# Optimization experiments

Measured on AMD Instinct MI355X. Metric: run time of the kernel, lower is better.

Reference implementation:

```python
import jax, jax.numpy as jnp
import numpy as np

HEADS = 16

def rotate_half(x):
    x1, x2 = jnp.split(x, 2, axis=-1)
    return jnp.concatenate((-x2, x1), axis=-1)

def setup_inputs() -> dict:
    key = jax.random.key(0)
    k1, k2, k3, k4 = jax.random.split(key, 4)
    b, n, h = 2, 2048, 1024
    d = h // HEADS
    x = jax.random.normal(k1, (b, n, h), dtype=jnp.float32)
    rotary_emb = jax.random.normal(k2, (n, d), dtype=jnp.float32)
    w_qkv = jax.random.normal(k3, (h, 3 * h), dtype=jnp.float32) * (1.0 / np.sqrt(h))
    w_out = jax.random.normal(k4, (h, h), dtype=jnp.float32) * (1.0 / np.sqrt(h))
    return {"x": x, "rotary_emb": rotary_emb, "w_qkv": w_qkv, "w_out": w_out}

def reference(x, rotary_emb, w_qkv, w_out):
    b, n, hidden = x.shape
    d = hidden // HEADS
    # fused QKV projection: [b,n,3*hidden]
    qkv = jnp.einsum('bnh,hk->bnk', x, w_qkv)
    q, k, v = jnp.split(qkv, 3, axis=-1)
    # [b,n,hidden] -> [b,H,n,d]
    split_heads = lambda t: t.reshape(b, n, HEADS, d).transpose(0, 2, 1, 3)
    q, k, v = split_heads(q), split_heads(k), split_heads(v)
    # rotary: pos is [n,d], broadcast over batch/heads
    cos = jnp.cos(rotary_emb)[None, None]
    sin = jnp.sin(rotary_emb)[None, None]
    q = q * cos + rotate_half(q) * sin
    k = k * cos + rotate_half(k) * sin
    # SDPA (no mask, no dropout)
    scale = 1.0 / np.sqrt(d).astype(np.float32)
    scores = jnp.einsum('bhqd,bhkd->bhqk', q, k) * scale
    attn = jax.nn.softmax(scores, axis=-1)
    out = jnp.einsum('bhqk,bhkd->bhqd', attn, v)
    out = out.transpose(0, 2, 1, 3).reshape(b, n, hidden)
    return jnp.einsum('bnh,hk->bnk', out, w_out)
```

## Files before the change

kernel.cpp:

```cpp
#include <hip/hip_runtime.h>
#include <math.h>

#define HEADS 16
#define DH    64
#define SEQ   2048
#define HID   1024
#define NROW  4096

typedef __attribute__((ext_vector_type(8))) short bf16x8;
typedef __attribute__((ext_vector_type(4))) float f32x4;

#define AS1 __attribute__((address_space(1)))
#define AS3 __attribute__((address_space(3)))

#define QSCALE 0.18033688011112042f

__device__ __forceinline__ unsigned short f2bf(float x) {
    unsigned int u = __builtin_bit_cast(unsigned int, x);
    u = (u + 0x7FFFu + ((u >> 16) & 1u)) >> 16;
    return (unsigned short)u;
}

__device__ __forceinline__ void gload_lds16(const unsigned short* g, unsigned short* l) {
    __builtin_amdgcn_global_load_lds((AS1 void*)g, (AS3 void*)l, 16, 0, 0);
}

__device__ void wtrans_body(const float* __restrict__ wsrc, unsigned short* __restrict__ wt,
                            int K, int N, int bx, int by, float (*T)[65])
{
    const int tid = threadIdx.x;
    const int k0 = by * 64, n0 = bx * 64;
    #pragma unroll
    for (int rnd = 0; rnd < 4; ++rnd) {
        int row = (tid >> 4) + rnd * 16;
        int c = (tid & 15) * 4;
        float4 v = *(const float4*)&wsrc[(size_t)(k0 + row) * N + n0 + c];
        T[row][c] = v.x; T[row][c+1] = v.y; T[row][c+2] = v.z; T[row][c+3] = v.w;
    }
    __syncthreads();
    const int sr = tid >> 3, sc = (tid & 7) << 3;
    #pragma unroll
    for (int half = 0; half < 2; ++half) {
        int n = sr + half * 32;
        union { unsigned short u[8]; bf16x8 v; } pk;
        #pragma unroll
        for (int j = 0; j < 8; ++j) pk.u[j] = f2bf(T[sc + j][n]);
        *(bf16x8*)&wt[(size_t)(n0 + n) * K + k0 + sc] = pk.v;
    }
}

__global__ __launch_bounds__(256) void prep(const float* __restrict__ x,
                                            const float* __restrict__ rot,
                                            const float* __restrict__ w_qkv,
                                            const float* __restrict__ w_out,
                                            unsigned short* __restrict__ xb,
                                            float2* __restrict__ ctab,
                                            unsigned short* __restrict__ wqkvT,
                                            unsigned short* __restrict__ woutT)
{
    __shared__ float T[64][65];
    const int bid = blockIdx.x;
    if (bid < 2048) {
        size_t i = ((size_t)bid * 256 + threadIdx.x) * 8;
        float4 a = *(const float4*)&x[i];
        float4 b = *(const float4*)&x[i + 4];
        union { unsigned short u[8]; bf16x8 v; } pk;
        pk.u[0] = f2bf(a.x); pk.u[1] = f2bf(a.y); pk.u[2] = f2bf(a.z); pk.u[3] = f2bf(a.w);
        pk.u[4] = f2bf(b.x); pk.u[5] = f2bf(b.y); pk.u[6] = f2bf(b.z); pk.u[7] = f2bf(b.w);
        *(bf16x8*)&xb[i] = pk.v;
    } else if (bid < 2560) {
        int i = (bid - 2048) * 256 + threadIdx.x;
        float r = rot[i];
        float s, c;
        __sincosf(r, &s, &c);
        ctab[i] = make_float2(c, s);
    } else if (bid < 3328) {
        int idx = bid - 2560;
        wtrans_body(w_qkv, wqkvT, 1024, 3072, idx % 48, idx / 48, T);
    } else {
        int idx = bid - 3328;
        wtrans_body(w_out, woutT, 1024, 1024, idx % 16, idx / 16, T);
    }
}

__global__ __launch_bounds__(256) void gemm_qkv(const unsigned short* __restrict__ A,
                                                const unsigned short* __restrict__ Bt,
                                                const float2* __restrict__ ctab,
                                                unsigned short* __restrict__ qb,
                                                unsigned short* __restrict__ kb,
                                                unsigned short* __restrict__ vt)
{
    __shared__ __align__(16) unsigned short As[128 * 32];
    __shared__ __align__(16) unsigned short Bs[128 * 32];
    const int tid = threadIdx.x;
    const int w = tid >> 6, lane = tid & 63;
    const int quad = lane >> 4, lm = lane & 15;
    const int wr = (w >> 1) * 64, wc = (w & 1) * 64;
    const int bm = blockIdx.y * 128, bn = blockIdx.x * 128;
    const int m0 = tid >> 2;
    const int sk = (tid & 3) << 3;

    f32x4 acc[4][4];
    #pragma unroll
    for (int i = 0; i < 4; ++i)
        #pragma unroll
        for (int j = 0; j < 4; ++j) acc[i][j] = (f32x4){0.f, 0.f, 0.f, 0.f};

    for (int k0 = 0; k0 < 1024; k0 += 32) {
        __syncthreads();
        gload_lds16(&A [(size_t)(bm + m0     ) * 1024 + k0 + sk], As + (size_t)w * 512);
        gload_lds16(&A [(size_t)(bm + m0 + 64) * 1024 + k0 + sk], As + 2048 + (size_t)w * 512);
        gload_lds16(&Bt[(size_t)(bn + m0     ) * 1024 + k0 + sk], Bs + (size_t)w * 512);
        gload_lds16(&Bt[(size_t)(bn + m0 + 64) * 1024 + k0 + sk], Bs + 2048 + (size_t)w * 512);
        __syncthreads();
        bf16x8 af[4], bfr[4];
        #pragma unroll
        for (int mt = 0; mt < 4; ++mt) af[mt] = *(const bf16x8*)&As[(wr + mt * 16 + lm) * 32 + quad * 8];
        #pragma unroll
        for (int nt = 0; nt < 4; ++nt) bfr[nt] = *(const bf16x8*)&Bs[(wc + nt * 16 + lm) * 32 + quad * 8];
        #pragma unroll
        for (int mt = 0; mt < 4; ++mt)
            #pragma unroll
            for (int nt = 0; nt < 4; ++nt)
                acc[mt][nt] = __builtin_amdgcn_mfma_f32_16x16x32_bf16(af[mt], bfr[nt], acc[mt][nt], 0, 0, 0);
    }

    const int colbase = bn + wc;
    const int region = colbase >> 10;
    const int h = (colbase >> 6) & 15;

    if (region == 2) {
        #pragma unroll
        for (int mt = 0; mt < 4; ++mt) {
            int rowb = bm + wr + mt * 16 + quad * 4;
            int b = rowb >> 11, seq = rowb & (SEQ - 1);
            int t = seq >> 5, ks = seq & 31;
            #pragma unroll
            for (int nt = 0; nt < 4; ++nt) {
                int d = nt * 16 + lm;
                ushort4 pk;
                pk.x = f2bf(acc[mt][nt][0]); pk.y = f2bf(acc[mt][nt][1]);
                pk.z = f2bf(acc[mt][nt][2]); pk.w = f2bf(acc[mt][nt][3]);
                *(ushort4*)&vt[(((size_t)(b * HEADS + h) * 64 + t) * 64 + d) * 32 + ks] = pk;
            }
        }
    } else {
        const float qs = (region == 0) ? QSCALE : 1.0f;
        unsigned short* dst = (region == 0) ? qb : kb;
        #pragma unroll
        for (int mt = 0; mt < 4; ++mt) {
            #pragma unroll
            for (int nt = 0; nt < 2; ++nt) {
                int d = nt * 16 + lm;
                #pragma unroll
                for (int r = 0; r < 4; ++r) {
                    int row = bm + wr + mt * 16 + quad * 4 + r;
                    int b = row >> 11, seq = row & (SEQ - 1);
                    float2 cs0 = ctab[seq * DH + d];
                    float2 cs1 = ctab[seq * DH + d + 32];
                    float x0 = acc[mt][nt][r];
                    float x1 = acc[mt][nt + 2][r];
                    size_t ob = ((size_t)(b * HEADS + h) * SEQ + seq) * DH;
                    dst[ob + d]      = f2bf((x0 * cs0.x - x1 * cs0.y) * qs);
                    dst[ob + d + 32] = f2bf((x1 * cs1.x + x0 * cs1.y) * qs);
                }
            }
        }
    }
}

#define PSW 36
#define OPW 68
__global__ __launch_bounds__(256, 3) void attn6(const unsigned short* __restrict__ qb,
                                                const unsigned short* __restrict__ kb,
                                                const unsigned short* __restrict__ vt,
                                                unsigned short* __restrict__ attnb)
{
    __shared__ __align__(16) char smem[4 * 64 * PSW * 2];
    unsigned short* Ps   = (unsigned short*)smem;
    float*          oBuf = (float*)smem;
    float*          lRed = (float*)(smem + 17408);

    const int tid = threadIdx.x;
    const int w = tid >> 6, lane = tid & 63, quad = lane >> 4, lm = lane & 15;
    const int bh = blockIdx.y, q0 = blockIdx.x * 64;
    const int b = bh >> 4, h = bh & 15;
    const size_t hb = (size_t)bh * SEQ * DH;
    unsigned short* myPs = Ps + w * (64 * PSW);

    bf16x8 qf[4][2];
    #pragma unroll
    for (int qt = 0; qt < 4; ++qt)
        #pragma unroll
        for (int c = 0; c < 2; ++c)
            qf[qt][c] = *(const bf16x8*)&qb[hb + (size_t)(q0 + qt * 16 + lm) * DH + c * 32 + quad * 8];

    float rs[4] = {0.f, 0.f, 0.f, 0.f};
    f32x4 o[4][4];
    #pragma unroll
    for (int qt = 0; qt < 4; ++qt)
        #pragma unroll
        for (int dt = 0; dt < 4; ++dt) o[qt][dt] = (f32x4){0.f, 0.f, 0.f, 0.f};

    const unsigned short* kp = kb + hb + (size_t)(w * 512 + lm) * DH + quad * 8;
    const unsigned short* vp = vt + (((size_t)bh * 64 + w * 16) * 64 + lm) * 32 + quad * 8;

    #pragma unroll 4
    for (int it = 0; it < 16; ++it) {
        bf16x8 kf[2][2];
        #pragma unroll
        for (int kt = 0; kt < 2; ++kt)
            #pragma unroll
            for (int c = 0; c < 2; ++c)
                kf[kt][c] = *(const bf16x8*)(kp + kt * 1024 + c * 32);
        bf16x8 vf[4];
        #pragma unroll
        for (int dt = 0; dt < 4; ++dt)
            vf[dt] = *(const bf16x8*)(vp + dt * 512);

        #pragma unroll
        for (int kt = 0; kt < 2; ++kt) {
            f32x4 s[4];
            #pragma unroll
            for (int qt = 0; qt < 4; ++qt) {
                f32x4 z = (f32x4){0.f, 0.f, 0.f, 0.f};
                z = __builtin_amdgcn_mfma_f32_16x16x32_bf16(kf[kt][0], qf[qt][0], z, 0, 0, 0);
                s[qt] = __builtin_amdgcn_mfma_f32_16x16x32_bf16(kf[kt][1], qf[qt][1], z, 0, 0, 0);
            }
            #pragma unroll
            for (int qt = 0; qt < 4; ++qt) {
                unsigned int u[4];
                #pragma unroll
                for (int r = 0; r < 4; ++r) {
                    float p = __builtin_amdgcn_exp2f(s[qt][r]);
                    rs[qt] += p;
                    u[r] = __builtin_bit_cast(unsigned int, p);
                }
                unsigned int lo = __builtin_amdgcn_perm(u[1], u[0], 0x07060302);
                unsigned int hi = __builtin_amdgcn_perm(u[3], u[2], 0x07060302);
                unsigned long long pv = ((unsigned long long)hi << 32) | lo;
                *(unsigned long long*)&myPs[(qt * 16 + lm) * PSW + kt * 16 + quad * 4] = pv;
            }
        }
        #pragma unroll
        for (int qt = 0; qt < 4; ++qt) {
            bf16x8 pf = *(const bf16x8*)&myPs[(qt * 16 + lm) * PSW + quad * 8];
            #pragma unroll
            for (int dt = 0; dt < 4; ++dt)
                o[qt][dt] = __builtin_amdgcn_mfma_f32_16x16x32_bf16(pf, vf[dt], o[qt][dt], 0, 0, 0);
        }
        kp += 2048;
        vp += 2048;
    }

    #pragma unroll
    for (int off = 16; off < 64; off <<= 1)
        #pragma unroll
        for (int qt = 0; qt < 4; ++qt) rs[qt] += __shfl_xor(rs[qt], off, 64);

    __syncthreads();
    if (w > 0 && quad == 0) {
        #pragma unroll
        for (int qt = 0; qt < 4; ++qt) lRed[(w - 1) * 64 + qt * 16 + lm] = rs[qt];
    }
    __syncthreads();
    if (w == 0) {
        #pragma unroll
        for (int qt = 0; qt < 4; ++qt)
            rs[qt] += lRed[qt * 16 + lm] + lRed[64 + qt * 16 + lm] + lRed[128 + qt * 16 + lm];
    }
    #pragma unroll
    for (int s = 1; s < 4; ++s) {
        __syncthreads();
        if (w == s) {
            #pragma unroll
            for (int qt = 0; qt < 4; ++qt)
                #pragma unroll
                for (int dt = 0; dt < 4; ++dt)
                    #pragma unroll
                    for (int r = 0; r < 4; ++r)
                        oBuf[(qt * 16 + quad * 4 + r) * OPW + dt * 16 + lm] = o[qt][dt][r];
        }
        __syncthreads();
        if (w == 0) {
            #pragma unroll
            for (int qt = 0; qt < 4; ++qt)
                #pragma unroll
                for (int dt = 0; dt < 4; ++dt)
                    #pragma unroll
                    for (int r = 0; r < 4; ++r)
                        o[qt][dt][r] += oBuf[(qt * 16 + quad * 4 + r) * OPW + dt * 16 + lm];
        }
    }
    if (w == 0) {
        #pragma unroll
        for (int qt = 0; qt < 4; ++qt)
            #pragma unroll
            for (int r = 0; r < 4; ++r) {
                float inv = 1.0f / __shfl(rs[qt], quad * 4 + r, 64);
                int row = b * SEQ + q0 + qt * 16 + quad * 4 + r;
                #pragma unroll
                for (int dt = 0; dt < 4; ++dt)
                    attnb[(size_t)row * HID + h * DH + dt * 16 + lm] = f2bf(o[qt][dt][r] * inv);
            }
    }
}

__global__ __launch_bounds__(256) void gemm_out(const unsigned short* __restrict__ A,
                                                const unsigned short* __restrict__ Bt,
                                                float* __restrict__ C)
{
    __shared__ __align__(16) unsigned short As[64 * 32];
    __shared__ __align__(16) unsigned short Bs[128 * 32];
    const int tid = threadIdx.x;
    const int w = tid >> 6, lane = tid & 63;
    const int quad = lane >> 4, lm = lane & 15;
    const int wr = (w >> 1) * 32, wc = (w & 1) * 64;
    const int bm = blockIdx.y * 64, bn = blockIdx.x * 128;
    const int m0 = tid >> 2;
    const int sk = (tid & 3) << 3;

    f32x4 acc[2][4];
    #pragma unroll
    for (int i = 0; i < 2; ++i)
        #pragma unroll
        for (int j = 0; j < 4; ++j) acc[i][j] = (f32x4){0.f, 0.f, 0.f, 0.f};

    for (int k0 = 0; k0 < 1024; k0 += 32) {
        __syncthreads();
        gload_lds16(&A [(size_t)(bm + m0     ) * 1024 + k0 + sk], As + (size_t)w * 512);
        gload_lds16(&Bt[(size_t)(bn + m0     ) * 1024 + k0 + sk], Bs + (size_t)w * 512);
        gload_lds16(&Bt[(size_t)(bn + m0 + 64) * 1024 + k0 + sk], Bs + 2048 + (size_t)w * 512);
        __syncthreads();
        bf16x8 af[2], bfr[4];
        #pragma unroll
        for (int mt = 0; mt < 2; ++mt) af[mt] = *(const bf16x8*)&As[(wr + mt * 16 + lm) * 32 + quad * 8];
        #pragma unroll
        for (int nt = 0; nt < 4; ++nt) bfr[nt] = *(const bf16x8*)&Bs[(wc + nt * 16 + lm) * 32 + quad * 8];
        #pragma unroll
        for (int mt = 0; mt < 2; ++mt)
            #pragma unroll
            for (int nt = 0; nt < 4; ++nt)
                acc[mt][nt] = __builtin_amdgcn_mfma_f32_16x16x32_bf16(af[mt], bfr[nt], acc[mt][nt], 0, 0, 0);
    }

    #pragma unroll
    for (int mt = 0; mt < 2; ++mt)
        #pragma unroll
        for (int nt = 0; nt < 4; ++nt) {
            int col = bn + wc + nt * 16 + lm;
            #pragma unroll
            for (int r = 0; r < 4; ++r) {
                int row = bm + wr + mt * 16 + quad * 4 + r;
                C[(size_t)row * 1024 + col] = acc[mt][nt][r];
            }
        }
}

extern "C" void kernel_launch(void* const* d_in, const int* in_sizes, int n_in,
                              void* d_out, int out_size, void* d_ws, size_t ws_size,
                              hipStream_t stream) {
    const float* x     = (const float*)d_in[0];
    const float* rot   = (const float*)d_in[1];
    const float* w_qkv = (const float*)d_in[2];
    const float* w_out = (const float*)d_in[3];
    float* out = (float*)d_out;

    char* ws = (char*)d_ws;
    unsigned short* xb    = (unsigned short*)(ws);
    unsigned short* qb    = (unsigned short*)(ws + (size_t)( 8u << 20));
    unsigned short* kb    = (unsigned short*)(ws + (size_t)(16u << 20));
    unsigned short* vt    = (unsigned short*)(ws + (size_t)(24u << 20));
    unsigned short* attnb = (unsigned short*)(ws + (size_t)(32u << 20));
    unsigned short* wqkvT = (unsigned short*)(ws + (size_t)(40u << 20));
    unsigned short* woutT = (unsigned short*)(ws + (size_t)(46u << 20));
    float2*         ctab  = (float2*)        (ws + (size_t)(48u << 20));

    prep<<<3584, 256, 0, stream>>>(x, rot, w_qkv, w_out, xb, ctab, wqkvT, woutT);

    gemm_qkv<<<dim3(24, 32), 256, 0, stream>>>(xb, wqkvT, ctab, qb, kb, vt);

    attn6<<<dim3(SEQ / 64, 32), 256, 0, stream>>>(qb, kb, vt, attnb);

    gemm_out<<<dim3(8, 64), 256, 0, stream>>>(attnb, woutT, out);
}
```

Before: 211.8 us.

## Stage K/V tiles in LDS with double-buffered async loads, 128-query blocks

The attention kernel now processes 128 queries per block, split across two query groups and two key groups of waves, instead of 64 queries with four key-split waves. K and V tiles are streamed into shared memory through double-buffered global_load_lds with an XOR swizzle, so all waves in a block share each fetched tile rather than each wave reading K/V from global memory. The final cross-wave reduction shrinks to a single pairwise merge. In exchange, LDS use grows to about 50KB, occupancy is lowered to 2 blocks per SM, a barrier is added each iteration, and the grid is halved.

```diff
diff --git a/kernel.cpp b/kernel.cpp
--- a/kernel.cpp
+++ b/kernel.cpp
@@ -169,31 +169,51 @@
     }
 }
 
-#define PSW 36
-#define OPW 68
-__global__ __launch_bounds__(256, 3) void attn6(const unsigned short* __restrict__ qb,
+#define PSW9 36
+__global__ __launch_bounds__(256, 2) void attn9(const unsigned short* __restrict__ qb,
                                                 const unsigned short* __restrict__ kb,
                                                 const unsigned short* __restrict__ vt,
                                                 unsigned short* __restrict__ attnb)
 {
-    __shared__ __align__(16) char smem[4 * 64 * PSW * 2];
-    unsigned short* Ps   = (unsigned short*)smem;
-    float*          oBuf = (float*)smem;
-    float*          lRed = (float*)(smem + 17408);
+    __shared__ __align__(16) char smem[51200];
+    unsigned short* Ks = (unsigned short*)smem;
+    unsigned short* Vs = (unsigned short*)(smem + 16384);
+    unsigned short* Ps = (unsigned short*)(smem + 32768);
 
     const int tid = threadIdx.x;
     const int w = tid >> 6, lane = tid & 63, quad = lane >> 4, lm = lane & 15;
-    const int bh = blockIdx.y, q0 = blockIdx.x * 64;
+    const int qg = w >> 1, kg = w & 1;
+    const int bh = blockIdx.y, q0 = blockIdx.x * 128;
     const int b = bh >> 4, h = bh & 15;
     const size_t hb = (size_t)bh * SEQ * DH;
-    unsigned short* myPs = Ps + w * (64 * PSW);
+    unsigned short* myPs = Ps + w * (64 * PSW9);
 
     bf16x8 qf[4][2];
     #pragma unroll
     for (int qt = 0; qt < 4; ++qt)
         #pragma unroll
         for (int c = 0; c < 2; ++c)
-            qf[qt][c] = *(const bf16x8*)&qb[hb + (size_t)(q0 + qt * 16 + lm) * DH + c * 32 + quad * 8];
+            qf[qt][c] = *(const bf16x8*)&qb[hb + (size_t)(q0 + qg * 64 + qt * 16 + lm) * DH + c * 32 + quad * 8];
+
+    const int r0 = (w * 16) + (lane >> 3);
+    const int p0 = lane & 7;
+    const int gk0 = r0 * 64 + (p0 ^ (r0 & 7)) * 8;
+    const int r1 = r0 + 8;
+    const int gk1 = r1 * 64 + (p0 ^ (r1 & 7)) * 8;
+    const unsigned short* kgp = kb + hb;
+    const unsigned short* vgp = vt + hb;
+    const int gv0 = w * 1024 + lane * 8;
+    const int gv1 = gv0 + 512;
+    unsigned short* kdst0 = Ks + w * 1024;
+    unsigned short* kdst1 = Ks + w * 1024 + 512;
+    unsigned short* vdst0 = Vs + w * 1024;
+    unsigned short* vdst1 = Vs + w * 1024 + 512;
+
+    int kfo[2];
+    #pragma unroll
+    for (int c = 0; c < 2; ++c)
+        kfo[c] = (kg * 32 + lm) * 64 + (((c * 4 + quad) ^ (lm & 7)) * 8);
+    const int vfo = kg * 2048 + lm * 32 + quad * 8;
 
     float rs[4] = {0.f, 0.f, 0.f, 0.f};
     f32x4 o[4][4];
@@ -202,30 +222,41 @@
         #pragma unroll
         for (int dt = 0; dt < 4; ++dt) o[qt][dt] = (f32x4){0.f, 0.f, 0.f, 0.f};
 
-    const unsigned short* kp = kb + hb + (size_t)(w * 512 + lm) * DH + quad * 8;
-    const unsigned short* vp = vt + (((size_t)bh * 64 + w * 16) * 64 + lm) * 32 + quad * 8;
-
-    #pragma unroll 4
-    for (int it = 0; it < 16; ++it) {
-        bf16x8 kf[2][2];
-        #pragma unroll
-        for (int kt = 0; kt < 2; ++kt)
-            #pragma unroll
-            for (int c = 0; c < 2; ++c)
-                kf[kt][c] = *(const bf16x8*)(kp + kt * 1024 + c * 32);
+    gload_lds16(kgp + gk0, kdst0);
+    gload_lds16(kgp + gk1, kdst1);
+    gload_lds16(vgp + gv0, vdst0);
+    gload_lds16(vgp + gv1, vdst1);
+
+    #pragma unroll 2
+    for (int it = 0; it < 32; ++it) {
+        const int buf = it & 1;
+        __syncthreads();
+        {
+            const size_t nb = (size_t)((it + 1) & 31) * 4096;
+            const int bo = (buf ^ 1) * 4096;
+            gload_lds16(kgp + nb + gk0, kdst0 + bo);
+            gload_lds16(kgp + nb + gk1, kdst1 + bo);
+            gload_lds16(vgp + nb + gv0, vdst0 + bo);
+            gload_lds16(vgp + nb + gv1, vdst1 + bo);
+        }
+        const unsigned short* Kb = Ks + buf * 4096;
+        const unsigned short* Vb = Vs + buf * 4096;
+
         bf16x8 vf[4];
         #pragma unroll
         for (int dt = 0; dt < 4; ++dt)
-            vf[dt] = *(const bf16x8*)(vp + dt * 512);
+            vf[dt] = *(const bf16x8*)&Vb[vfo + dt * 512];
 
         #pragma unroll
         for (int kt = 0; kt < 2; ++kt) {
+            bf16x8 k0 = *(const bf16x8*)&Kb[kfo[0] + kt * 1024];
+            bf16x8 k1 = *(const bf16x8*)&Kb[kfo[1] + kt * 1024];
             f32x4 s[4];
             #pragma unroll
             for (int qt = 0; qt < 4; ++qt) {
                 f32x4 z = (f32x4){0.f, 0.f, 0.f, 0.f};
-                z = __builtin_amdgcn_mfma_f32_16x16x32_bf16(kf[kt][0], qf[qt][0], z, 0, 0, 0);
-                s[qt] = __builtin_amdgcn_mfma_f32_16x16x32_bf16(kf[kt][1], qf[qt][1], z, 0, 0, 0);
+                z = __builtin_amdgcn_mfma_f32_16x16x32_bf16(k0, qf[qt][0], z, 0, 0, 0);
+                s[qt] = __builtin_amdgcn_mfma_f32_16x16x32_bf16(k1, qf[qt][1], z, 0, 0, 0);
             }
             #pragma unroll
             for (int qt = 0; qt < 4; ++qt) {
@@ -239,18 +270,16 @@
                 unsigned int lo = __builtin_amdgcn_perm(u[1], u[0], 0x07060302);
                 unsigned int hi = __builtin_amdgcn_perm(u[3], u[2], 0x07060302);
                 unsigned long long pv = ((unsigned long long)hi << 32) | lo;
-                *(unsigned long long*)&myPs[(qt * 16 + lm) * PSW + kt * 16 + quad * 4] = pv;
+                *(unsigned long long*)&myPs[(qt * 16 + lm) * PSW9 + kt * 16 + quad * 4] = pv;
             }
         }
         #pragma unroll
         for (int qt = 0; qt < 4; ++qt) {
-            bf16x8 pf = *(const bf16x8*)&myPs[(qt * 16 + lm) * PSW + quad * 8];
+            bf16x8 pf = *(const bf16x8*)&myPs[(qt * 16 + lm) * PSW9 + quad * 8];
             #pragma unroll
             for (int dt = 0; dt < 4; ++dt)
                 o[qt][dt] = __builtin_amdgcn_mfma_f32_16x16x32_bf16(pf, vf[dt], o[qt][dt], 0, 0, 0);
         }
-        kp += 2048;
-        vp += 2048;
     }
 
     #pragma unroll
@@ -259,46 +288,38 @@
         for (int qt = 0; qt < 4; ++qt) rs[qt] += __shfl_xor(rs[qt], off, 64);
 
     __syncthreads();
-    if (w > 0 && quad == 0) {
-        #pragma unroll
-        for (int qt = 0; qt < 4; ++qt) lRed[(w - 1) * 64 + qt * 16 + lm] = rs[qt];
+    float* oBuf = (float*)smem;
+    float* lRed = (float*)(smem + 40960);
+    if (kg == 1) {
+        #pragma unroll
+        for (int qt = 0; qt < 4; ++qt)
+            #pragma unroll
+            for (int dt = 0; dt < 4; ++dt)
+                #pragma unroll
+                for (int r = 0; r < 4; ++r)
+                    oBuf[(qg * 64 + qt * 16 + quad * 4 + r) * 68 + dt * 16 + lm] = o[qt][dt][r];
+        if (quad == 0) {
+            #pragma unroll
+            for (int qt = 0; qt < 4; ++qt) lRed[qg * 64 + qt * 16 + lm] = rs[qt];
+        }
     }
     __syncthreads();
-    if (w == 0) {
-        #pragma unroll
-        for (int qt = 0; qt < 4; ++qt)
-            rs[qt] += lRed[qt * 16 + lm] + lRed[64 + qt * 16 + lm] + lRed[128 + qt * 16 + lm];
-    }
-    #pragma unroll
-    for (int s = 1; s < 4; ++s) {
-        __syncthreads();
-        if (w == s) {
-            #pragma unroll
-            for (int qt = 0; qt < 4; ++qt)
+    if (kg == 0) {
+        #pragma unroll
+        for (int qt = 0; qt < 4; ++qt) {
+            rs[qt] += lRed[qg * 64 + qt * 16 + lm];
+            #pragma unroll
+            for (int dt = 0; dt < 4; ++dt)
                 #pragma unroll
-                for (int dt = 0; dt < 4; ++dt)
-                    #pragma unroll
-                    for (int r = 0; r < 4; ++r)
-                        oBuf[(qt * 16 + quad * 4 + r) * OPW + dt * 16 + lm] = o[qt][dt][r];
-        }
-        __syncthreads();
-        if (w == 0) {
-            #pragma unroll
-            for (int qt = 0; qt < 4; ++qt)
-                #pragma unroll
-                for (int dt = 0; dt < 4; ++dt)
-                    #pragma unroll
-                    for (int r = 0; r < 4; ++r)
-                        o[qt][dt][r] += oBuf[(qt * 16 + quad * 4 + r) * OPW + dt * 16 + lm];
-        }
-    }
-    if (w == 0) {
+                for (int r = 0; r < 4; ++r)
+                    o[qt][dt][r] += oBuf[(qg * 64 + qt * 16 + quad * 4 + r) * 68 + dt * 16 + lm];
+        }
         #pragma unroll
         for (int qt = 0; qt < 4; ++qt)
             #pragma unroll
             for (int r = 0; r < 4; ++r) {
                 float inv = 1.0f / __shfl(rs[qt], quad * 4 + r, 64);
-                int row = b * SEQ + q0 + qt * 16 + quad * 4 + r;
+                int row = b * SEQ + q0 + qg * 64 + qt * 16 + quad * 4 + r;
                 #pragma unroll
                 for (int dt = 0; dt < 4; ++dt)
                     attnb[(size_t)row * HID + h * DH + dt * 16 + lm] = f2bf(o[qt][dt][r] * inv);
@@ -380,7 +401,7 @@
 
     gemm_qkv<<<dim3(24, 32), 256, 0, stream>>>(xb, wqkvT, ctab, qb, kb, vt);
 
-    attn6<<<dim3(SEQ / 64, 32), 256, 0, stream>>>(qb, kb, vt, attnb);
+    attn9<<<dim3(SEQ / 128, 32), 256, 0, stream>>>(qb, kb, vt, attnb);
 
     gemm_out<<<dim3(8, 64), 256, 0, stream>>>(attnb, woutT, out);
 }
```

Result: no change. 210.2 us (-0.8%).
